# Optimization experiments

Hardware: AMD Instinct MI355X
Metric: run time of the kernel (lower is better)

## Reference

```python
import jax, jax.numpy as jnp
import numpy as np

N, IN, HID, H, OUT = 5000, 64, 32, 4, 64
NEG_SLOPE = 0.2  # LeakyReLU slope used by GAT
MASK_VAL = -1e9


def setup_inputs() -> dict:
    key = jax.random.key(0)
    ks = jax.random.split(key, 8)
    adj = (jax.random.uniform(ks[0], (N, N)) < 0.02).astype(jnp.float32)
    adj = jnp.maximum(adj, jnp.eye(N, dtype=jnp.float32))
    h = jax.random.normal(ks[1], (N, IN), dtype=jnp.float32)
    # layer 1 params: W1 [IN, H*HID], attention vectors a1_* [H, HID]
    W1 = jax.random.normal(ks[2], (IN, H * HID), dtype=jnp.float32) / np.sqrt(IN)
    a1_src = jax.random.normal(ks[3], (H, HID), dtype=jnp.float32) / np.sqrt(HID)
    a1_dst = jax.random.normal(ks[4], (H, HID), dtype=jnp.float32) / np.sqrt(HID)
    # layer 2 params: single head, W2 [H*HID, OUT]
    W2 = jax.random.normal(ks[5], (H * HID, OUT), dtype=jnp.float32) / np.sqrt(H * HID)
    a2_src = jax.random.normal(ks[6], (1, OUT), dtype=jnp.float32) / np.sqrt(OUT)
    a2_dst = jax.random.normal(ks[7], (1, OUT), dtype=jnp.float32) / np.sqrt(OUT)
    return {"adj": adj, "h": h, "W1": W1, "a1_src": a1_src, "a1_dst": a1_dst,
            "W2": W2, "a2_src": a2_src, "a2_dst": a2_dst}


def gat_conv(adj, x, W, a_src, a_dst, heads, out_dim):
    n = x.shape[0]
    Wh = (x @ W).reshape(n, heads, out_dim)              # [N, H, F']
    s_src = jnp.einsum('nhf,hf->nh', Wh, a_src)          # score contribution of node as center i
    s_dst = jnp.einsum('nhf,hf->nh', Wh, a_dst)          # contribution of node as neighbor j
    e = s_src[:, None, :] + s_dst[None, :, :]            # [N, N, H]
    e = jax.nn.leaky_relu(e, NEG_SLOPE)
    e = jnp.where(adj[:, :, None] > 0, e, MASK_VAL)
    alpha = jax.nn.softmax(e, axis=1)                    # softmax over neighbors j
    out = jnp.einsum('ijh,jhf->ihf', alpha, Wh)          # aggregate
    return out.reshape(n, heads * out_dim)               # concat heads


def reference(adj, h, W1, a1_src, a1_dst, W2, a2_src, a2_dst):
    x = gat_conv(adj, h, W1, a1_src, a1_dst, H, HID)     # [N, H*HID]
    x = jax.nn.elu(x)
    out = gat_conv(adj, x, W2, a2_src, a2_dst, 1, OUT)   # [N, OUT]
    return out
```

## Files before the change

### kernel.cpp

```cpp
#include <hip/hip_runtime.h>
#include <math.h>

#define NN   5000
#define INF_ 64
#define HID  32
#define NH   4
#define OUTF 64
#define NEG  0.2f
#define CAP  256

__global__ __launch_bounds__(128) void k_wh1(const float* __restrict__ h,
        const float* __restrict__ W1, const float* __restrict__ a1s,
        const float* __restrict__ a1d, float* __restrict__ Wh1,
        float* __restrict__ s1s, float* __restrict__ s1d) {
    const int n = blockIdx.x, t = threadIdx.x;
    __shared__ float hs[INF_];
    if (t < INF_) hs[t] = h[n * INF_ + t];
    __syncthreads();
    float acc = 0.f;
#pragma unroll
    for (int k = 0; k < INF_; ++k) acc += hs[k] * W1[k * (NH * HID) + t];
    Wh1[n * (NH * HID) + t] = acc;
    const int hd = t >> 5, f = t & 31;
    float vs = acc * a1s[hd * HID + f];
    float vd = acc * a1d[hd * HID + f];
    for (int off = 16; off > 0; off >>= 1) {
        vs += __shfl_down(vs, off, 32);
        vd += __shfl_down(vd, off, 32);
    }
    if (f == 0) { s1s[n * NH + hd] = vs; s1d[n * NH + hd] = vd; }
}

__global__ __launch_bounds__(256) void k_csr(const float* __restrict__ adj,
        int* __restrict__ counts, int* __restrict__ idx) {
    const int i = blockIdx.x;
    __shared__ int cnt;
    if (threadIdx.x == 0) cnt = 0;
    __syncthreads();
    const float4* row4 = (const float4*)(adj + (size_t)i * NN);
    int* my = idx + (size_t)i * CAP;
    for (int j = threadIdx.x; j < NN / 4; j += 256) {
        float4 v = row4[j];
        if (v.x > 0.f) { int p = atomicAdd(&cnt, 1); if (p < CAP) my[p] = 4 * j + 0; }
        if (v.y > 0.f) { int p = atomicAdd(&cnt, 1); if (p < CAP) my[p] = 4 * j + 1; }
        if (v.z > 0.f) { int p = atomicAdd(&cnt, 1); if (p < CAP) my[p] = 4 * j + 2; }
        if (v.w > 0.f) { int p = atomicAdd(&cnt, 1); if (p < CAP) my[p] = 4 * j + 3; }
    }
    __syncthreads();
    if (threadIdx.x == 0) counts[i] = cnt < CAP ? cnt : CAP;
}

__global__ __launch_bounds__(128) void k_attn1(const int* __restrict__ counts,
        const int* __restrict__ idx, const float* __restrict__ Wh1,
        const float* __restrict__ s1s, const float* __restrict__ s1d,
        float* __restrict__ x) {
    const int i = blockIdx.x, t = threadIdx.x;
    const int c = counts[i];
    __shared__ int   nb[CAP];
    __shared__ float sc[CAP * NH];
    __shared__ float red[NH * 128];
    for (int e = t; e < c; e += 128) nb[e] = idx[(size_t)i * CAP + e];
    __syncthreads();
    float ssrc[NH];
#pragma unroll
    for (int hh = 0; hh < NH; ++hh) ssrc[hh] = s1s[i * NH + hh];
    for (int e = t; e < c; e += 128) {
        const int j = nb[e];
#pragma unroll
        for (int hh = 0; hh < NH; ++hh) {
            float v = ssrc[hh] + s1d[j * NH + hh];
            v = (v >= 0.f) ? v : NEG * v;
            sc[e * NH + hh] = v;
        }
    }
    __syncthreads();
    float lm[NH];
#pragma unroll
    for (int hh = 0; hh < NH; ++hh) lm[hh] = -1e30f;
    for (int e = t; e < c; e += 128)
#pragma unroll
        for (int hh = 0; hh < NH; ++hh) lm[hh] = fmaxf(lm[hh], sc[e * NH + hh]);
#pragma unroll
    for (int hh = 0; hh < NH; ++hh) red[hh * 128 + t] = lm[hh];
    __syncthreads();
    for (int s = 64; s > 0; s >>= 1) {
        if (t < s)
#pragma unroll
            for (int hh = 0; hh < NH; ++hh)
                red[hh * 128 + t] = fmaxf(red[hh * 128 + t], red[hh * 128 + t + s]);
        __syncthreads();
    }
    float m[NH];
#pragma unroll
    for (int hh = 0; hh < NH; ++hh) m[hh] = red[hh * 128];
    __syncthreads();
    float ls[NH];
#pragma unroll
    for (int hh = 0; hh < NH; ++hh) ls[hh] = 0.f;
    for (int e = t; e < c; e += 128)
#pragma unroll
        for (int hh = 0; hh < NH; ++hh) {
            float v = expf(sc[e * NH + hh] - m[hh]);
            sc[e * NH + hh] = v;
            ls[hh] += v;
        }
    __syncthreads();
#pragma unroll
    for (int hh = 0; hh < NH; ++hh) red[hh * 128 + t] = ls[hh];
    __syncthreads();
    for (int s = 64; s > 0; s >>= 1) {
        if (t < s)
#pragma unroll
            for (int hh = 0; hh < NH; ++hh)
                red[hh * 128 + t] += red[hh * 128 + t + s];
        __syncthreads();
    }
    float l[NH];
#pragma unroll
    for (int hh = 0; hh < NH; ++hh) l[hh] = red[hh * 128];
    const int hd = t >> 5;
    float acc = 0.f;
    for (int e = 0; e < c; ++e)
        acc += sc[e * NH + hd] * Wh1[(size_t)nb[e] * (NH * HID) + t];
    float o = acc / l[hd];
    o = (o > 0.f) ? o : expm1f(o);
    x[i * (NH * HID) + t] = o;
}

__global__ __launch_bounds__(64) void k_wh2(const float* __restrict__ x,
        const float* __restrict__ W2, const float* __restrict__ a2s,
        const float* __restrict__ a2d, float* __restrict__ Wh2,
        float* __restrict__ s2s, float* __restrict__ s2d) {
    const int n = blockIdx.x, t = threadIdx.x;
    __shared__ float xs[NH * HID];
    xs[t] = x[n * 128 + t];
    xs[t + 64] = x[n * 128 + 64 + t];
    __syncthreads();
    float acc = 0.f;
#pragma unroll
    for (int k = 0; k < 128; ++k) acc += xs[k] * W2[k * OUTF + t];
    Wh2[n * OUTF + t] = acc;
    float vs = acc * a2s[t];
    float vd = acc * a2d[t];
    for (int off = 32; off > 0; off >>= 1) {
        vs += __shfl_down(vs, off, 64);
        vd += __shfl_down(vd, off, 64);
    }
    if (t == 0) { s2s[n] = vs; s2d[n] = vd; }
}

__global__ __launch_bounds__(64) void k_attn2(const int* __restrict__ counts,
        const int* __restrict__ idx, const float* __restrict__ Wh2,
        const float* __restrict__ s2s, const float* __restrict__ s2d,
        float* __restrict__ out) {
    const int i = blockIdx.x, t = threadIdx.x;
    const int c = counts[i];
    __shared__ int   nb[CAP];
    __shared__ float sc[CAP];
    for (int e = t; e < c; e += 64) nb[e] = idx[(size_t)i * CAP + e];
    __syncthreads();
    const float si = s2s[i];
    float lm = -1e30f;
    for (int e = t; e < c; e += 64) {
        float v = si + s2d[nb[e]];
        v = (v >= 0.f) ? v : NEG * v;
        sc[e] = v;
        lm = fmaxf(lm, v);
    }
    for (int off = 32; off > 0; off >>= 1) lm = fmaxf(lm, __shfl_down(lm, off, 64));
    lm = __shfl(lm, 0, 64);
    float ls = 0.f;
    for (int e = t; e < c; e += 64) {
        float v = expf(sc[e] - lm);
        sc[e] = v;
        ls += v;
    }
    __syncthreads();
    for (int off = 32; off > 0; off >>= 1) ls += __shfl_down(ls, off, 64);
    ls = __shfl(ls, 0, 64);
    float acc = 0.f;
    for (int e = 0; e < c; ++e)
        acc += sc[e] * Wh2[(size_t)nb[e] * OUTF + t];
    out[i * OUTF + t] = acc / ls;
}

extern "C" void kernel_launch(void* const* d_in, const int* in_sizes, int n_in,
                              void* d_out, int out_size, void* d_ws, size_t ws_size,
                              hipStream_t stream) {
    const float* adj = (const float*)d_in[0];
    const float* h   = (const float*)d_in[1];
    const float* W1  = (const float*)d_in[2];
    const float* a1s = (const float*)d_in[3];
    const float* a1d = (const float*)d_in[4];
    const float* W2  = (const float*)d_in[5];
    const float* a2s = (const float*)d_in[6];
    const float* a2d = (const float*)d_in[7];
    float* out = (float*)d_out;

    char* p = (char*)d_ws;
    float* Wh1 = (float*)p; p += (size_t)NN * 128 * 4;
    float* xbuf= (float*)p; p += (size_t)NN * 128 * 4;
    float* Wh2 = (float*)p; p += (size_t)NN * OUTF * 4;
    float* s1s = (float*)p; p += (size_t)NN * NH * 4;
    float* s1d = (float*)p; p += (size_t)NN * NH * 4;
    float* s2s = (float*)p; p += (size_t)NN * 4;
    float* s2d = (float*)p; p += (size_t)NN * 4;
    int*   cnt = (int*)p;   p += (size_t)NN * 4;
    int*   idx = (int*)p;   p += (size_t)NN * CAP * 4;

    k_csr  <<<NN, 256, 0, stream>>>(adj, cnt, idx);
    k_wh1  <<<NN, 128, 0, stream>>>(h, W1, a1s, a1d, Wh1, s1s, s1d);
    k_attn1<<<NN, 128, 0, stream>>>(cnt, idx, Wh1, s1s, s1d, xbuf);
    k_wh2  <<<NN,  64, 0, stream>>>(xbuf, W2, a2s, a2d, Wh2, s2s, s2d);
    k_attn2<<<NN,  64, 0, stream>>>(cnt, idx, Wh2, s2s, s2d, out);
}
```

Measured before the change: 209.3 us.

## Fuse five GAT kernels into three with wider blocks and split aggregation

Merges CSR construction with the layer-1 projection, and attention-1 with the layer-2 projection, so the x buffer round trip and two launches disappear. The adjacency scan now uses nontemporal loads. Attention kernels move to 256 threads with wave-shuffle reductions in place of shared-memory tree reductions. The neighbor aggregation is split across waves with 4-way unrolled independent accumulators to expose more memory-level parallelism. The trade-off is larger blocks, more shared memory and extra syncs per block.

```diff
diff --git a/kernel.cpp b/kernel.cpp
--- a/kernel.cpp
+++ b/kernel.cpp
@@ -9,179 +9,219 @@
 #define NEG  0.2f
 #define CAP  256
 
-__global__ __launch_bounds__(128) void k_wh1(const float* __restrict__ h,
-        const float* __restrict__ W1, const float* __restrict__ a1s,
-        const float* __restrict__ a1d, float* __restrict__ Wh1,
-        float* __restrict__ s1s, float* __restrict__ s1d) {
-    const int n = blockIdx.x, t = threadIdx.x;
+typedef float nt4 __attribute__((ext_vector_type(4)));
+
+__device__ inline float wred_max(float v) {
+#pragma unroll
+    for (int off = 32; off > 0; off >>= 1) v = fmaxf(v, __shfl_down(v, off, 64));
+    return v;
+}
+__device__ inline float wred_sum(float v) {
+#pragma unroll
+    for (int off = 32; off > 0; off >>= 1) v += __shfl_down(v, off, 64);
+    return v;
+}
+
+__global__ __launch_bounds__(256) void k1(const float* __restrict__ adj,
+        const float* __restrict__ h, const float* __restrict__ W1,
+        const float* __restrict__ a1s, const float* __restrict__ a1d,
+        int* __restrict__ counts, int* __restrict__ idx,
+        float* __restrict__ Wh1, float* __restrict__ s1s, float* __restrict__ s1d) {
+    const int i = blockIdx.x, t = threadIdx.x;
+    __shared__ int cnt;
     __shared__ float hs[INF_];
-    if (t < INF_) hs[t] = h[n * INF_ + t];
-    __syncthreads();
-    float acc = 0.f;
-#pragma unroll
-    for (int k = 0; k < INF_; ++k) acc += hs[k] * W1[k * (NH * HID) + t];
-    Wh1[n * (NH * HID) + t] = acc;
-    const int hd = t >> 5, f = t & 31;
-    float vs = acc * a1s[hd * HID + f];
-    float vd = acc * a1d[hd * HID + f];
-    for (int off = 16; off > 0; off >>= 1) {
-        vs += __shfl_down(vs, off, 32);
-        vd += __shfl_down(vd, off, 32);
-    }
-    if (f == 0) { s1s[n * NH + hd] = vs; s1d[n * NH + hd] = vd; }
-}
-
-__global__ __launch_bounds__(256) void k_csr(const float* __restrict__ adj,
-        int* __restrict__ counts, int* __restrict__ idx) {
-    const int i = blockIdx.x;
-    __shared__ int cnt;
-    if (threadIdx.x == 0) cnt = 0;
-    __syncthreads();
-    const float4* row4 = (const float4*)(adj + (size_t)i * NN);
+    if (t == 0) cnt = 0;
+    if (t < INF_) hs[t] = h[i * INF_ + t];
+    __syncthreads();
+    const nt4* row4 = (const nt4*)(adj + (size_t)i * NN);
     int* my = idx + (size_t)i * CAP;
-    for (int j = threadIdx.x; j < NN / 4; j += 256) {
-        float4 v = row4[j];
+    for (int j = t; j < NN / 4; j += 256) {
+        nt4 v = __builtin_nontemporal_load(&row4[j]);
         if (v.x > 0.f) { int p = atomicAdd(&cnt, 1); if (p < CAP) my[p] = 4 * j + 0; }
         if (v.y > 0.f) { int p = atomicAdd(&cnt, 1); if (p < CAP) my[p] = 4 * j + 1; }
         if (v.z > 0.f) { int p = atomicAdd(&cnt, 1); if (p < CAP) my[p] = 4 * j + 2; }
         if (v.w > 0.f) { int p = atomicAdd(&cnt, 1); if (p < CAP) my[p] = 4 * j + 3; }
     }
-    __syncthreads();
-    if (threadIdx.x == 0) counts[i] = cnt < CAP ? cnt : CAP;
-}
-
-__global__ __launch_bounds__(128) void k_attn1(const int* __restrict__ counts,
+    if (t < 128) {
+        float acc = 0.f;
+#pragma unroll
+        for (int k = 0; k < INF_; ++k) acc += hs[k] * W1[k * (NH * HID) + t];
+        Wh1[(size_t)i * (NH * HID) + t] = acc;
+        const int hd = t >> 5, f = t & 31;
+        float vs = acc * a1s[hd * HID + f];
+        float vd = acc * a1d[hd * HID + f];
+#pragma unroll
+        for (int off = 16; off > 0; off >>= 1) {
+            vs += __shfl_down(vs, off, 32);
+            vd += __shfl_down(vd, off, 32);
+        }
+        if (f == 0) { s1s[i * NH + hd] = vs; s1d[i * NH + hd] = vd; }
+    }
+    __syncthreads();
+    if (t == 0) counts[i] = cnt < CAP ? cnt : CAP;
+}
+
+__global__ __launch_bounds__(256) void k2(const int* __restrict__ counts,
         const int* __restrict__ idx, const float* __restrict__ Wh1,
         const float* __restrict__ s1s, const float* __restrict__ s1d,
-        float* __restrict__ x) {
+        const float* __restrict__ W2, const float* __restrict__ a2s,
+        const float* __restrict__ a2d, float* __restrict__ Wh2,
+        float* __restrict__ s2s, float* __restrict__ s2d) {
     const int i = blockIdx.x, t = threadIdx.x;
+    const int lane = t & 63, wave = t >> 6;
     const int c = counts[i];
     __shared__ int   nb[CAP];
-    __shared__ float sc[CAP * NH];
-    __shared__ float red[NH * 128];
-    for (int e = t; e < c; e += 128) nb[e] = idx[(size_t)i * CAP + e];
+    __shared__ float sc[NH][CAP];
+    __shared__ float xs[128];
+    __shared__ float agg[128];
+    __shared__ float redh[4 * NH];
+    __shared__ float mh[NH], lh[NH];
+    __shared__ float pw[4][64];
+    for (int e = t; e < c; e += 256) nb[e] = idx[(size_t)i * CAP + e];
     __syncthreads();
     float ssrc[NH];
 #pragma unroll
     for (int hh = 0; hh < NH; ++hh) ssrc[hh] = s1s[i * NH + hh];
-    for (int e = t; e < c; e += 128) {
+    float lm[NH] = {-1e30f, -1e30f, -1e30f, -1e30f};
+    for (int e = t; e < c; e += 256) {
         const int j = nb[e];
 #pragma unroll
         for (int hh = 0; hh < NH; ++hh) {
             float v = ssrc[hh] + s1d[j * NH + hh];
             v = (v >= 0.f) ? v : NEG * v;
-            sc[e * NH + hh] = v;
+            sc[hh][e] = v;
+            lm[hh] = fmaxf(lm[hh], v);
         }
     }
-    __syncthreads();
-    float lm[NH];
-#pragma unroll
-    for (int hh = 0; hh < NH; ++hh) lm[hh] = -1e30f;
-    for (int e = t; e < c; e += 128)
-#pragma unroll
-        for (int hh = 0; hh < NH; ++hh) lm[hh] = fmaxf(lm[hh], sc[e * NH + hh]);
-#pragma unroll
-    for (int hh = 0; hh < NH; ++hh) red[hh * 128 + t] = lm[hh];
-    __syncthreads();
-    for (int s = 64; s > 0; s >>= 1) {
-        if (t < s)
-#pragma unroll
-            for (int hh = 0; hh < NH; ++hh)
-                red[hh * 128 + t] = fmaxf(red[hh * 128 + t], red[hh * 128 + t + s]);
-        __syncthreads();
-    }
-    float m[NH];
-#pragma unroll
-    for (int hh = 0; hh < NH; ++hh) m[hh] = red[hh * 128];
-    __syncthreads();
-    float ls[NH];
-#pragma unroll
-    for (int hh = 0; hh < NH; ++hh) ls[hh] = 0.f;
-    for (int e = t; e < c; e += 128)
+#pragma unroll
+    for (int hh = 0; hh < NH; ++hh) {
+        float v = wred_max(lm[hh]);
+        if (lane == 0) redh[wave * NH + hh] = v;
+    }
+    __syncthreads();
+    if (t < NH) {
+        float m = redh[t];
+#pragma unroll
+        for (int w = 1; w < 4; ++w) m = fmaxf(m, redh[w * NH + t]);
+        mh[t] = m;
+    }
+    __syncthreads();
+    float lsum[NH] = {0.f, 0.f, 0.f, 0.f};
+    for (int e = t; e < c; e += 256) {
 #pragma unroll
         for (int hh = 0; hh < NH; ++hh) {
-            float v = expf(sc[e * NH + hh] - m[hh]);
-            sc[e * NH + hh] = v;
-            ls[hh] += v;
+            float v = expf(sc[hh][e] - mh[hh]);
+            sc[hh][e] = v;
+            lsum[hh] += v;
         }
-    __syncthreads();
-#pragma unroll
-    for (int hh = 0; hh < NH; ++hh) red[hh * 128 + t] = ls[hh];
-    __syncthreads();
-    for (int s = 64; s > 0; s >>= 1) {
-        if (t < s)
-#pragma unroll
-            for (int hh = 0; hh < NH; ++hh)
-                red[hh * 128 + t] += red[hh * 128 + t + s];
-        __syncthreads();
-    }
-    float l[NH];
-#pragma unroll
-    for (int hh = 0; hh < NH; ++hh) l[hh] = red[hh * 128];
-    const int hd = t >> 5;
-    float acc = 0.f;
-    for (int e = 0; e < c; ++e)
-        acc += sc[e * NH + hd] * Wh1[(size_t)nb[e] * (NH * HID) + t];
-    float o = acc / l[hd];
-    o = (o > 0.f) ? o : expm1f(o);
-    x[i * (NH * HID) + t] = o;
-}
-
-__global__ __launch_bounds__(64) void k_wh2(const float* __restrict__ x,
-        const float* __restrict__ W2, const float* __restrict__ a2s,
-        const float* __restrict__ a2d, float* __restrict__ Wh2,
-        float* __restrict__ s2s, float* __restrict__ s2d) {
-    const int n = blockIdx.x, t = threadIdx.x;
-    __shared__ float xs[NH * HID];
-    xs[t] = x[n * 128 + t];
-    xs[t + 64] = x[n * 128 + 64 + t];
-    __syncthreads();
-    float acc = 0.f;
-#pragma unroll
-    for (int k = 0; k < 128; ++k) acc += xs[k] * W2[k * OUTF + t];
-    Wh2[n * OUTF + t] = acc;
-    float vs = acc * a2s[t];
-    float vd = acc * a2d[t];
-    for (int off = 32; off > 0; off >>= 1) {
-        vs += __shfl_down(vs, off, 64);
-        vd += __shfl_down(vd, off, 64);
-    }
-    if (t == 0) { s2s[n] = vs; s2d[n] = vd; }
-}
-
-__global__ __launch_bounds__(64) void k_attn2(const int* __restrict__ counts,
+    }
+#pragma unroll
+    for (int hh = 0; hh < NH; ++hh) {
+        float v = wred_sum(lsum[hh]);
+        if (lane == 0) redh[wave * NH + hh] = v;
+    }
+    __syncthreads();
+    if (t < NH) lh[t] = redh[t] + redh[NH + t] + redh[2 * NH + t] + redh[3 * NH + t];
+    __syncthreads();
+    const int chunk = t >> 7, f = t & 127, hd = f >> 5;
+    const int half = (((c + 1) >> 1) + 3) & ~3;
+    const int e0 = chunk * half;
+    const int e1 = min(c, e0 + half);
+    float a0 = 0.f, a1 = 0.f, a2 = 0.f, a3 = 0.f;
+    int e = e0;
+    for (; e + 3 < e1; e += 4) {
+        int j0 = nb[e], j1 = nb[e + 1], j2 = nb[e + 2], j3 = nb[e + 3];
+        a0 += sc[hd][e]     * Wh1[(size_t)j0 * 128 + f];
+        a1 += sc[hd][e + 1] * Wh1[(size_t)j1 * 128 + f];
+        a2 += sc[hd][e + 2] * Wh1[(size_t)j2 * 128 + f];
+        a3 += sc[hd][e + 3] * Wh1[(size_t)j3 * 128 + f];
+    }
+    for (; e < e1; ++e) a0 += sc[hd][e] * Wh1[(size_t)nb[e] * 128 + f];
+    float acc = (a0 + a1) + (a2 + a3);
+    if (chunk == 0) agg[f] = acc;
+    __syncthreads();
+    if (chunk == 1) agg[f] += acc;
+    __syncthreads();
+    if (t < 128) {
+        float o = agg[t] / lh[t >> 5];
+        o = (o > 0.f) ? o : expm1f(o);
+        xs[t] = o;
+    }
+    __syncthreads();
+    {
+        float pa = 0.f;
+#pragma unroll
+        for (int k = 0; k < 32; ++k)
+            pa += xs[wave * 32 + k] * W2[(wave * 32 + k) * OUTF + lane];
+        pw[wave][lane] = pa;
+    }
+    __syncthreads();
+    if (t < 64) {
+        float w = pw[0][t] + pw[1][t] + pw[2][t] + pw[3][t];
+        Wh2[(size_t)i * OUTF + t] = w;
+        float vs = wred_sum(w * a2s[t]);
+        float vd = wred_sum(w * a2d[t]);
+        if (t == 0) { s2s[i] = vs; s2d[i] = vd; }
+    }
+}
+
+__global__ __launch_bounds__(256) void k3(const int* __restrict__ counts,
         const int* __restrict__ idx, const float* __restrict__ Wh2,
         const float* __restrict__ s2s, const float* __restrict__ s2d,
         float* __restrict__ out) {
     const int i = blockIdx.x, t = threadIdx.x;
+    const int lane = t & 63, wave = t >> 6;
     const int c = counts[i];
     __shared__ int   nb[CAP];
     __shared__ float sc[CAP];
-    for (int e = t; e < c; e += 64) nb[e] = idx[(size_t)i * CAP + e];
+    __shared__ float red[4];
+    __shared__ float ms_, ls_;
+    __shared__ float agg[4][64];
+    for (int e = t; e < c; e += 256) nb[e] = idx[(size_t)i * CAP + e];
     __syncthreads();
     const float si = s2s[i];
     float lm = -1e30f;
-    for (int e = t; e < c; e += 64) {
+    for (int e = t; e < c; e += 256) {
         float v = si + s2d[nb[e]];
         v = (v >= 0.f) ? v : NEG * v;
         sc[e] = v;
         lm = fmaxf(lm, v);
     }
-    for (int off = 32; off > 0; off >>= 1) lm = fmaxf(lm, __shfl_down(lm, off, 64));
-    lm = __shfl(lm, 0, 64);
-    float ls = 0.f;
-    for (int e = t; e < c; e += 64) {
-        float v = expf(sc[e] - lm);
+    lm = wred_max(lm);
+    if (lane == 0) red[wave] = lm;
+    __syncthreads();
+    if (t == 0) ms_ = fmaxf(fmaxf(red[0], red[1]), fmaxf(red[2], red[3]));
+    __syncthreads();
+    const float m = ms_;
+    float lsum = 0.f;
+    for (int e = t; e < c; e += 256) {
+        float v = expf(sc[e] - m);
         sc[e] = v;
-        ls += v;
-    }
-    __syncthreads();
-    for (int off = 32; off > 0; off >>= 1) ls += __shfl_down(ls, off, 64);
-    ls = __shfl(ls, 0, 64);
-    float acc = 0.f;
-    for (int e = 0; e < c; ++e)
-        acc += sc[e] * Wh2[(size_t)nb[e] * OUTF + t];
-    out[i * OUTF + t] = acc / ls;
+        lsum += v;
+    }
+    lsum = wred_sum(lsum);
+    if (lane == 0) red[wave] = lsum;
+    __syncthreads();
+    if (t == 0) ls_ = red[0] + red[1] + red[2] + red[3];
+    __syncthreads();
+    const int q = (((c + 3) >> 2) + 3) & ~3;
+    const int e0 = wave * q;
+    const int e1 = min(c, e0 + q);
+    float a0 = 0.f, a1 = 0.f, a2 = 0.f, a3 = 0.f;
+    int e = e0;
+    for (; e + 3 < e1; e += 4) {
+        a0 += sc[e]     * Wh2[(size_t)nb[e]     * OUTF + lane];
+        a1 += sc[e + 1] * Wh2[(size_t)nb[e + 1] * OUTF + lane];
+        a2 += sc[e + 2] * Wh2[(size_t)nb[e + 2] * OUTF + lane];
+        a3 += sc[e + 3] * Wh2[(size_t)nb[e + 3] * OUTF + lane];
+    }
+    for (; e < e1; ++e) a0 += sc[e] * Wh2[(size_t)nb[e] * OUTF + lane];
+    agg[wave][lane] = (a0 + a1) + (a2 + a3);
+    __syncthreads();
+    if (t < 64) {
+        float s = agg[0][t] + agg[1][t] + agg[2][t] + agg[3][t];
+        out[(size_t)i * OUTF + t] = s / ls_;
+    }
 }
 
 extern "C" void kernel_launch(void* const* d_in, const int* in_sizes, int n_in,
@@ -199,7 +239,6 @@
 
     char* p = (char*)d_ws;
     float* Wh1 = (float*)p; p += (size_t)NN * 128 * 4;
-    float* xbuf= (float*)p; p += (size_t)NN * 128 * 4;
     float* Wh2 = (float*)p; p += (size_t)NN * OUTF * 4;
     float* s1s = (float*)p; p += (size_t)NN * NH * 4;
     float* s1d = (float*)p; p += (size_t)NN * NH * 4;
@@ -208,9 +247,7 @@
     int*   cnt = (int*)p;   p += (size_t)NN * 4;
     int*   idx = (int*)p;   p += (size_t)NN * CAP * 4;
 
-    k_csr  <<<NN, 256, 0, stream>>>(adj, cnt, idx);
-    k_wh1  <<<NN, 128, 0, stream>>>(h, W1, a1s, a1d, Wh1, s1s, s1d);
-    k_attn1<<<NN, 128, 0, stream>>>(cnt, idx, Wh1, s1s, s1d, xbuf);
-    k_wh2  <<<NN,  64, 0, stream>>>(xbuf, W2, a2s, a2d, Wh2, s2s, s2d);
-    k_attn2<<<NN,  64, 0, stream>>>(cnt, idx, Wh2, s2s, s2d, out);
-}
+    k1<<<NN, 256, 0, stream>>>(adj, h, W1, a1s, a1d, cnt, idx, Wh1, s1s, s1d);
+    k2<<<NN, 256, 0, stream>>>(cnt, idx, Wh1, s1s, s1d, W2, a2s, a2d, Wh2, s2s, s2d);
+    k3<<<NN, 256, 0, stream>>>(cnt, idx, Wh2, s2s, s2d, out);
+}
```

Result: no change. 212.0 us (+1.3%).
